# Kernel tuning notes

Measured on AMD Instinct MI355X. Metric: run time of the kernel, lower is better.

Reference implementation:

```python
import jax, jax.numpy as jnp
import numpy as np

N, IN_CH, HID, OUT = 3072, 128, 256, 32
HEADS = 12


def setup_inputs() -> dict:
    key = jax.random.key(0)
    ks = jax.random.split(key, 16)

    def glorot(k, shape):
        fan_in, fan_out = shape[0], shape[-1]
        lim = float(np.sqrt(6.0 / (fan_in + fan_out)))
        return jax.random.uniform(k, shape, jnp.float32, -lim, lim)

    return {
        "x": jax.random.normal(ks[0], (N, IN_CH), jnp.float32),
        "attn_tensor": jax.random.normal(ks[1], (HEADS, N, N), jnp.float32),
        "edge_weight": jnp.ones((1,), jnp.float32),  # unused (use_edge_weight=False)
        "batch_idx": jnp.zeros((N,), jnp.int64),      # single graph
        # Conv2d(12,1,1) == per-head scalar mix
        "agg_w": jax.random.normal(ks[2], (HEADS,), jnp.float32) * 0.1,
        "agg_b": jnp.zeros((1,), jnp.float32),
        # GCNConv weights (x @ W then propagate, + bias)
        "W1": glorot(ks[3], (IN_CH, HID)), "b1": jnp.zeros((HID,), jnp.float32),
        "W2": glorot(ks[4], (HID, HID)),   "b2": jnp.zeros((HID,), jnp.float32),
        # final MLP: Linear -> ReLU -> LayerNorm -> Linear
        "lin1_W": glorot(ks[5], (HID, HID)), "lin1_b": jnp.zeros((HID,), jnp.float32),
        "ln_g": jnp.ones((HID,), jnp.float32), "ln_b": jnp.zeros((HID,), jnp.float32),
        "lin2_W": glorot(ks[6], (HID, OUT)), "lin2_b": jnp.zeros((OUT,), jnp.float32),
    }


def reference(x, attn_tensor, edge_weight, batch_idx,
              agg_w, agg_b, W1, b1, W2, b2,
              lin1_W, lin1_b, ln_g, ln_b, lin2_W, lin2_b):
    threshold = 0.0
    n = x.shape[0]

    # Conv2d(12,1,kernel_size=1): weighted sum over heads -> [N, N] score matrix
    agg = jnp.einsum('c,cij->ij', agg_w, attn_tensor) + agg_b[0]

    # thresholded adjacency (mask.nonzero() -> edge_index), kept dense in jax
    A = (agg > threshold).astype(x.dtype)  # A[s, t] = edge s->t

    # PyG gcn_norm with add_remaining_self_loops (binary weights -> diag = 1)
    eye = jnp.eye(n, dtype=x.dtype)
    A_hat = A * (1.0 - eye) + eye
    deg = A_hat.sum(axis=0)                        # in-degree at target nodes
    dinv = jnp.where(deg > 0, jax.lax.rsqrt(deg), 0.0)
    A_norm = dinv[:, None] * A_hat * dinv[None, :]  # norm = dinv[src] * dinv[dst]

    # GCNConv 1: out[t] = sum_s A_norm[s,t] (x W)[s] + b
    h = jnp.einsum('st,sd->td', A_norm, x @ W1) + b1
    h = jax.nn.relu(h)
    # GCNConv 2
    h = jnp.einsum('st,sd->td', A_norm, h @ W2) + b2

    # global_mean_pool over batch_idx (single graph here)
    bi = batch_idx.astype(jnp.int32)
    sums = jax.ops.segment_sum(h, bi, num_segments=1)
    counts = jax.ops.segment_sum(jnp.ones((n,), h.dtype), bi, num_segments=1)
    g = sums / counts[:, None]

    # Linear -> ReLU -> LayerNorm -> Linear
    z = jax.nn.relu(g @ lin1_W + lin1_b)
    mu = z.mean(axis=-1, keepdims=True)
    var = ((z - mu) ** 2).mean(axis=-1, keepdims=True)
    z = (z - mu) * jax.lax.rsqrt(var + 1e-5) * ln_g + ln_b
    out = z @ lin2_W + lin2_b
    return out
```

## Files before the change

kernel.cpp:

```cpp
#include <hip/hip_runtime.h>
#include <hip/hip_bf16.h>

#define NN     3072
#define NWORDS 48
#define INCH   128
#define HID    256
#define NHEADS 12
#define PLANE  9437184LL

typedef __attribute__((ext_vector_type(8))) short     s16x8;
typedef __attribute__((ext_vector_type(4))) float     f32x4;
typedef __attribute__((ext_vector_type(8))) unsigned short u16x8;

__device__ inline unsigned short bf16_rne(float f) {
    unsigned int u = __float_as_uint(f);
    u += 0x7FFFu + ((u >> 16) & 1u);
    return (unsigned short)(u >> 16);
}

__global__ __launch_bounds__(256) void k_adj(const float* __restrict__ attn,
                                             const float* __restrict__ agg_w,
                                             const float* __restrict__ agg_b,
                                             unsigned long long* __restrict__ mask,
                                             unsigned long long* __restrict__ maskT) {
    __shared__ unsigned short chunk[4][64];
    const int w = threadIdx.x >> 6, l = threadIdx.x & 63;
    const int t0 = (blockIdx.x % 48) * 64;
    const int s0 = (blockIdx.x / 48) * 64;
    const int t = t0 + l;

    float wc[NHEADS];
#pragma unroll
    for (int c = 0; c < NHEADS; ++c) wc[c] = agg_w[c];
    const float bias = agg_b[0];

    unsigned int colchunk = 0;
#pragma unroll 2
    for (int i = 0; i < 16; ++i) {
        const int s = s0 + w * 16 + i;
        const float* p = attn + (long long)s * NN + t;
        float acc = bias;
#pragma unroll
        for (int c = 0; c < NHEADS; ++c)
            acc = fmaf(wc[c], p[(long long)c * PLANE], acc);
        bool pred = (acc > 0.0f) || (s == t);
        unsigned long long word = __ballot(pred);
        if (l == 0) mask[s * NWORDS + (t0 >> 6)] = word;
        colchunk |= (pred ? 1u : 0u) << i;
    }
    chunk[w][l] = (unsigned short)colchunk;
    __syncthreads();
    if (threadIdx.x < 64) {
        unsigned long long m = (unsigned long long)chunk[0][threadIdx.x]
                             | ((unsigned long long)chunk[1][threadIdx.x] << 16)
                             | ((unsigned long long)chunk[2][threadIdx.x] << 32)
                             | ((unsigned long long)chunk[3][threadIdx.x] << 48);
        maskT[(long long)(t0 + threadIdx.x) * NWORDS + (s0 >> 6)] = m;
    }
}

__global__ __launch_bounds__(256) void k_dinv(const unsigned long long* __restrict__ maskT,
                                              float* __restrict__ dinv,
                                              unsigned short* __restrict__ dinvb) {
    int t = blockIdx.x * 256 + threadIdx.x;
    const unsigned long long* row = maskT + (long long)t * NWORDS;
    int deg = 0;
#pragma unroll
    for (int w = 0; w < NWORDS; ++w) deg += __popcll(row[w]);
    float di = rsqrtf((float)deg);
    dinv[t] = di;
    dinvb[t] = bf16_rne(di);
}

__global__ __launch_bounds__(256) void k_fused(const unsigned long long* __restrict__ mask,
                                               const float* __restrict__ dinv,
                                               const float* __restrict__ x,
                                               const float* __restrict__ W1,
                                               float* __restrict__ w2sum,
                                               unsigned short* __restrict__ y1t) {
    if (blockIdx.x < 768) {
        const int w = threadIdx.x >> 6, l = threadIdx.x & 63;
        const int s = blockIdx.x * 4 + w;
        unsigned long long myword = (l < NWORDS) ? mask[s * NWORDS + l] : 0ULL;
        float acc = 0.0f;
#pragma unroll 8
        for (int j = 0; j < NWORDS; ++j) {
            unsigned long long wj = __shfl(myword, j);
            float dv = dinv[j * 64 + l];
            acc += ((wj >> l) & 1ULL) ? dv : 0.0f;
        }
#pragma unroll
        for (int o = 1; o < 64; o <<= 1) acc += __shfl_xor(acc, o);
        if (l == 0) w2sum[s] = dinv[s] * acc;
    } else {
        __shared__ float xs[8][INCH];
        int s0 = (blockIdx.x - 768) * 8;
        for (int i = threadIdx.x; i < 8 * INCH; i += 256)
            xs[i >> 7][i & 127] = x[s0 * INCH + i];
        __syncthreads();
        int d = threadIdx.x;
        float acc[8] = {0, 0, 0, 0, 0, 0, 0, 0};
        for (int k = 0; k < INCH; ++k) {
            float w = W1[k * HID + d];
#pragma unroll
            for (int r = 0; r < 8; ++r) acc[r] = fmaf(xs[r][k], w, acc[r]);
        }
        u16x8 v;
#pragma unroll
        for (int r = 0; r < 8; ++r) v[r] = bf16_rne(acc[r]);
        *(u16x8*)(y1t + (long long)d * NN + s0) = v;
    }
}

__global__ __launch_bounds__(256) void k_prop(const unsigned long long* __restrict__ maskT,
                                              const unsigned short* __restrict__ dinvb,
                                              const unsigned short* __restrict__ y1t,
                                              float* __restrict__ partials) {
    const int w = threadIdx.x >> 6, l = threadIdx.x & 63;
    const int lr = l & 15, lg = l >> 4;
    const int t0 = blockIdx.x * 64 + w * 16;
    const int d0 = blockIdx.y * 128;
    const int z  = blockIdx.z;

    const unsigned long long* mrow = maskT + (long long)(t0 + lr) * NWORDS + z * 12;

    const unsigned short* B[8];
#pragma unroll
    for (int n = 0; n < 8; ++n)
        B[n] = y1t + (long long)(d0 + n * 16 + lr) * NN;

    f32x4 acc[8];
#pragma unroll
    for (int n = 0; n < 8; ++n) acc[n] = (f32x4){0.f, 0.f, 0.f, 0.f};

#pragma unroll 2
    for (int kw = 0; kw < 12; ++kw) {
        unsigned long long word = mrow[kw];
#pragma unroll
        for (int half = 0; half < 2; ++half) {
            const int k0 = z * 768 + kw * 64 + half * 32 + lg * 8;
            unsigned int bits = (unsigned int)((word >> (half * 32 + lg * 8)) & 0xFFULL);
            u16x8 dv = *(const u16x8*)(dinvb + k0);
            s16x8 av;
#pragma unroll
            for (int j = 0; j < 8; ++j)
                av[j] = ((bits >> j) & 1u) ? (short)dv[j] : (short)0;
#pragma unroll
            for (int n = 0; n < 8; ++n) {
                s16x8 bv = *(const s16x8*)(const void*)(B[n] + k0);
                acc[n] = __builtin_amdgcn_mfma_f32_16x16x32_bf16(av, bv, acc[n], 0, 0, 0);
            }
        }
    }

    const int trow = t0 + lg * 4;
#pragma unroll
    for (int n = 0; n < 8; ++n) {
        const int d = d0 + n * 16 + lr;
#pragma unroll
        for (int r = 0; r < 4; ++r)
            partials[((size_t)z * NN + trow + r) * HID + d] = acc[n][r];
    }
}

__global__ __launch_bounds__(256) void k_vred(const float* __restrict__ partials,
                                              const float* __restrict__ dinv,
                                              const float* __restrict__ b1,
                                              const float* __restrict__ w2sum,
                                              float* __restrict__ vp) {
    const int b = blockIdx.x, d = threadIdx.x;
    const float bb = b1[d];
    float vacc = 0.0f;
#pragma unroll
    for (int i = 0; i < 8; ++i) {
        const int t = b * 8 + i;
        float ssum = partials[((size_t)0 * NN + t) * HID + d]
                   + partials[((size_t)1 * NN + t) * HID + d]
                   + partials[((size_t)2 * NN + t) * HID + d]
                   + partials[((size_t)3 * NN + t) * HID + d];
        float h = fmaxf(fmaf(dinv[t], ssum, bb), 0.0f);
        vacc = fmaf(w2sum[t], h, vacc);
    }
    vp[b * HID + d] = vacc;
}

__global__ __launch_bounds__(256) void k_head(const float* __restrict__ vp,
                                              const float* __restrict__ W2,
                                              const float* __restrict__ b2,
                                              const float* __restrict__ l1W,
                                              const float* __restrict__ l1b,
                                              const float* __restrict__ lng,
                                              const float* __restrict__ lnb,
                                              const float* __restrict__ l2W,
                                              const float* __restrict__ l2b,
                                              float* __restrict__ out) {
    __shared__ float vs[HID], gs[HID], zs[HID], red[4];
    int d = threadIdx.x;
    float v = 0.0f;
    for (int c = 0; c < 384; ++c) v += vp[c * HID + d];
    vs[d] = v;
    __syncthreads();
    float a = 0.0f;
    for (int k = 0; k < HID; ++k) a = fmaf(vs[k], W2[k * HID + d], a);
    gs[d] = b2[d] + a * (1.0f / 3072.0f);
    __syncthreads();
    float z1 = l1b[d];
    for (int k = 0; k < HID; ++k) z1 = fmaf(gs[k], l1W[k * HID + d], z1);
    z1 = fmaxf(z1, 0.0f);
    float sum = z1;
    for (int o = 1; o < 64; o <<= 1) sum += __shfl_xor(sum, o);
    if ((d & 63) == 0) red[d >> 6] = sum;
    __syncthreads();
    float mu = (red[0] + red[1] + red[2] + red[3]) * (1.0f / 256.0f);
    __syncthreads();
    float diff = z1 - mu, sq = diff * diff;
    for (int o = 1; o < 64; o <<= 1) sq += __shfl_xor(sq, o);
    if ((d & 63) == 0) red[d >> 6] = sq;
    __syncthreads();
    float var = (red[0] + red[1] + red[2] + red[3]) * (1.0f / 256.0f);
    float zn = diff * rsqrtf(var + 1e-5f) * lng[d] + lnb[d];
    zs[d] = zn;
    __syncthreads();
    if (d < 32) {
        float o = l2b[d];
        for (int k = 0; k < HID; ++k) o = fmaf(zs[k], l2W[k * 32 + d], o);
        out[d] = o;
    }
}

extern "C" void kernel_launch(void* const* d_in, const int* in_sizes, int n_in,
                              void* d_out, int out_size, void* d_ws, size_t ws_size,
                              hipStream_t stream) {
    const float* x     = (const float*)d_in[0];
    const float* attn  = (const float*)d_in[1];
    const float* agg_w = (const float*)d_in[4];
    const float* agg_b = (const float*)d_in[5];
    const float* W1    = (const float*)d_in[6];
    const float* b1    = (const float*)d_in[7];
    const float* W2    = (const float*)d_in[8];
    const float* b2    = (const float*)d_in[9];
    const float* l1W   = (const float*)d_in[10];
    const float* l1b   = (const float*)d_in[11];
    const float* lng   = (const float*)d_in[12];
    const float* lnb   = (const float*)d_in[13];
    const float* l2W   = (const float*)d_in[14];
    const float* l2b   = (const float*)d_in[15];
    float* out = (float*)d_out;

    char* ws = (char*)d_ws;
    size_t off = 0;
    auto alloc = [&](size_t bytes) -> void* {
        off = (off + 255) & ~(size_t)255;
        void* p = ws + off;
        off += bytes;
        return p;
    };
    unsigned long long* mask  = (unsigned long long*)alloc((size_t)NN * NWORDS * 8);
    unsigned long long* maskT = (unsigned long long*)alloc((size_t)NN * NWORDS * 8);
    float*          dinv  = (float*)alloc((size_t)NN * 4);
    unsigned short* dinvb = (unsigned short*)alloc((size_t)NN * 2);
    float*          w2sum = (float*)alloc((size_t)NN * 4);
    unsigned short* y1t   = (unsigned short*)alloc((size_t)HID * NN * 2);
    float*          part  = (float*)alloc((size_t)4 * NN * HID * 4);
    float*          vp    = (float*)alloc((size_t)384 * HID * 4);

    hipLaunchKernelGGL(k_adj,   dim3(2304), dim3(256), 0, stream, attn, agg_w, agg_b, mask, maskT);
    hipLaunchKernelGGL(k_dinv,  dim3(12),   dim3(256), 0, stream, maskT, dinv, dinvb);
    hipLaunchKernelGGL(k_fused, dim3(1152), dim3(256), 0, stream, mask, dinv, x, W1, w2sum, y1t);
    hipLaunchKernelGGL(k_prop,  dim3(48, 2, 4), dim3(256), 0, stream, maskT, dinvb, y1t, part);
    hipLaunchKernelGGL(k_vred,  dim3(384),  dim3(256), 0, stream, part, dinv, b1, w2sum, vp);
    hipLaunchKernelGGL(k_head,  dim3(1),    dim3(256), 0, stream,
                       vp, W2, b2, l1W, l1b, lng, lnb, l2W, l2b, out);
}
```

Before: 227.0 us.

## Drop row-major mask, vectorize adjacency build, fuse y1 and w2sum into other kernels

```diff
diff --git a/kernel.cpp b/kernel.cpp
--- a/kernel.cpp
+++ b/kernel.cpp
@@ -2,7 +2,7 @@
 #include <hip/hip_bf16.h>
 
 #define NN     3072
-#define NWORDS 48
+#define NW32   96
 #define INCH   128
 #define HID    256
 #define NHEADS 12
@@ -11,6 +11,7 @@
 typedef __attribute__((ext_vector_type(8))) short     s16x8;
 typedef __attribute__((ext_vector_type(4))) float     f32x4;
 typedef __attribute__((ext_vector_type(8))) unsigned short u16x8;
+typedef __attribute__((ext_vector_type(4))) unsigned int   u32x4;
 
 __device__ inline unsigned short bf16_rne(float f) {
     unsigned int u = __float_as_uint(f);
@@ -18,83 +19,59 @@
     return (unsigned short)(u >> 16);
 }
 
-__global__ __launch_bounds__(256) void k_adj(const float* __restrict__ attn,
-                                             const float* __restrict__ agg_w,
-                                             const float* __restrict__ agg_b,
-                                             unsigned long long* __restrict__ mask,
-                                             unsigned long long* __restrict__ maskT) {
-    __shared__ unsigned short chunk[4][64];
-    const int w = threadIdx.x >> 6, l = threadIdx.x & 63;
-    const int t0 = (blockIdx.x % 48) * 64;
-    const int s0 = (blockIdx.x / 48) * 64;
-    const int t = t0 + l;
-
-    float wc[NHEADS];
-#pragma unroll
-    for (int c = 0; c < NHEADS; ++c) wc[c] = agg_w[c];
-    const float bias = agg_b[0];
-
-    unsigned int colchunk = 0;
+__global__ __launch_bounds__(256) void k_adj_y1(const float* __restrict__ attn,
+                                                const float* __restrict__ agg_w,
+                                                const float* __restrict__ agg_b,
+                                                const float* __restrict__ x,
+                                                const float* __restrict__ W1,
+                                                unsigned int* __restrict__ maskT32,
+                                                unsigned short* __restrict__ y1t) {
+    __shared__ unsigned int chunkU[4][64];
+    __shared__ float xs[8][INCH];
+
+    if (blockIdx.x < 1152) {
+        const int w = threadIdx.x >> 6, l = threadIdx.x & 63;
+        const int t0 = (blockIdx.x % 12) * 256;
+        const int s0 = (blockIdx.x / 12) * 32;
+        const int tb = t0 + 4 * l;
+
+        float wc[NHEADS];
+#pragma unroll
+        for (int c = 0; c < NHEADS; ++c) wc[c] = agg_w[c];
+        const float bias = agg_b[0];
+
+        const float* base = attn + (long long)(s0 + 8 * w) * NN + tb;
+        unsigned int colb = 0;
 #pragma unroll 2
-    for (int i = 0; i < 16; ++i) {
-        const int s = s0 + w * 16 + i;
-        const float* p = attn + (long long)s * NN + t;
-        float acc = bias;
-#pragma unroll
-        for (int c = 0; c < NHEADS; ++c)
-            acc = fmaf(wc[c], p[(long long)c * PLANE], acc);
-        bool pred = (acc > 0.0f) || (s == t);
-        unsigned long long word = __ballot(pred);
-        if (l == 0) mask[s * NWORDS + (t0 >> 6)] = word;
-        colchunk |= (pred ? 1u : 0u) << i;
-    }
-    chunk[w][l] = (unsigned short)colchunk;
-    __syncthreads();
-    if (threadIdx.x < 64) {
-        unsigned long long m = (unsigned long long)chunk[0][threadIdx.x]
-                             | ((unsigned long long)chunk[1][threadIdx.x] << 16)
-                             | ((unsigned long long)chunk[2][threadIdx.x] << 32)
-                             | ((unsigned long long)chunk[3][threadIdx.x] << 48);
-        maskT[(long long)(t0 + threadIdx.x) * NWORDS + (s0 >> 6)] = m;
-    }
-}
-
-__global__ __launch_bounds__(256) void k_dinv(const unsigned long long* __restrict__ maskT,
-                                              float* __restrict__ dinv,
-                                              unsigned short* __restrict__ dinvb) {
-    int t = blockIdx.x * 256 + threadIdx.x;
-    const unsigned long long* row = maskT + (long long)t * NWORDS;
-    int deg = 0;
-#pragma unroll
-    for (int w = 0; w < NWORDS; ++w) deg += __popcll(row[w]);
-    float di = rsqrtf((float)deg);
-    dinv[t] = di;
-    dinvb[t] = bf16_rne(di);
-}
-
-__global__ __launch_bounds__(256) void k_fused(const unsigned long long* __restrict__ mask,
-                                               const float* __restrict__ dinv,
-                                               const float* __restrict__ x,
-                                               const float* __restrict__ W1,
-                                               float* __restrict__ w2sum,
-                                               unsigned short* __restrict__ y1t) {
-    if (blockIdx.x < 768) {
-        const int w = threadIdx.x >> 6, l = threadIdx.x & 63;
-        const int s = blockIdx.x * 4 + w;
-        unsigned long long myword = (l < NWORDS) ? mask[s * NWORDS + l] : 0ULL;
-        float acc = 0.0f;
-#pragma unroll 8
-        for (int j = 0; j < NWORDS; ++j) {
-            unsigned long long wj = __shfl(myword, j);
-            float dv = dinv[j * 64 + l];
-            acc += ((wj >> l) & 1ULL) ? dv : 0.0f;
-        }
-#pragma unroll
-        for (int o = 1; o < 64; o <<= 1) acc += __shfl_xor(acc, o);
-        if (l == 0) w2sum[s] = dinv[s] * acc;
+        for (int i = 0; i < 8; ++i) {
+            const int s = s0 + 8 * w + i;
+            const float* ps = base + (long long)i * NN;
+            f32x4 acc = {bias, bias, bias, bias};
+#pragma unroll
+            for (int c = 0; c < NHEADS; ++c) {
+                f32x4 v = *(const f32x4*)(ps + c * PLANE);
+                acc[0] = fmaf(wc[c], v[0], acc[0]);
+                acc[1] = fmaf(wc[c], v[1], acc[1]);
+                acc[2] = fmaf(wc[c], v[2], acc[2]);
+                acc[3] = fmaf(wc[c], v[3], acc[3]);
+            }
+            unsigned int bset = 0;
+            bset |= (acc[0] > 0.0f || s == tb + 0) ? (1u << i)        : 0u;
+            bset |= (acc[1] > 0.0f || s == tb + 1) ? (1u << (8 + i))  : 0u;
+            bset |= (acc[2] > 0.0f || s == tb + 2) ? (1u << (16 + i)) : 0u;
+            bset |= (acc[3] > 0.0f || s == tb + 3) ? (1u << (24 + i)) : 0u;
+            colb |= bset;
+        }
+        chunkU[w][l] = colb;
+        __syncthreads();
+        const int l2 = threadIdx.x >> 2, j = threadIdx.x & 3;
+        unsigned int word =  ((chunkU[0][l2] >> (8 * j)) & 0xFFu)
+                          | (((chunkU[1][l2] >> (8 * j)) & 0xFFu) << 8)
+                          | (((chunkU[2][l2] >> (8 * j)) & 0xFFu) << 16)
+                          | (((chunkU[3][l2] >> (8 * j)) & 0xFFu) << 24);
+        maskT32[(long long)(t0 + threadIdx.x) * NW32 + (s0 >> 5)] = word;
     } else {
-        __shared__ float xs[8][INCH];
-        int s0 = (blockIdx.x - 768) * 8;
+        int s0 = (blockIdx.x - 1152) * 8;
         for (int i = threadIdx.x; i < 8 * INCH; i += 256)
             xs[i >> 7][i & 127] = x[s0 * INCH + i];
         __syncthreads();
@@ -112,63 +89,112 @@
     }
 }
 
-__global__ __launch_bounds__(256) void k_prop(const unsigned long long* __restrict__ maskT,
+__global__ __launch_bounds__(256) void k_dinv(const unsigned int* __restrict__ maskT32,
+                                              float* __restrict__ dinv,
+                                              unsigned short* __restrict__ dinvb) {
+    int t = blockIdx.x * 256 + threadIdx.x;
+    const u32x4* row = (const u32x4*)(maskT32 + (long long)t * NW32);
+    int deg = 0;
+#pragma unroll
+    for (int i = 0; i < 24; ++i) {
+        u32x4 v = row[i];
+        deg += __popc(v[0]) + __popc(v[1]) + __popc(v[2]) + __popc(v[3]);
+    }
+    float di = rsqrtf((float)deg);
+    dinv[t] = di;
+    dinvb[t] = bf16_rne(di);
+}
+
+__global__ __launch_bounds__(256) void k_prop(const unsigned int* __restrict__ maskT32,
                                               const unsigned short* __restrict__ dinvb,
                                               const unsigned short* __restrict__ y1t,
-                                              float* __restrict__ partials) {
-    const int w = threadIdx.x >> 6, l = threadIdx.x & 63;
-    const int lr = l & 15, lg = l >> 4;
-    const int t0 = blockIdx.x * 64 + w * 16;
-    const int d0 = blockIdx.y * 128;
-    const int z  = blockIdx.z;
-
-    const unsigned long long* mrow = maskT + (long long)(t0 + lr) * NWORDS + z * 12;
-
-    const unsigned short* B[8];
-#pragma unroll
-    for (int n = 0; n < 8; ++n)
-        B[n] = y1t + (long long)(d0 + n * 16 + lr) * NN;
-
-    f32x4 acc[8];
-#pragma unroll
-    for (int n = 0; n < 8; ++n) acc[n] = (f32x4){0.f, 0.f, 0.f, 0.f};
+                                              const float* __restrict__ dinv,
+                                              float* __restrict__ partials,
+                                              float* __restrict__ w2p) {
+    if (blockIdx.x < 384) {
+        const int w = threadIdx.x >> 6, l = threadIdx.x & 63;
+        const int lr = l & 15, lg = l >> 4;
+        const int t0 = (blockIdx.x % 48) * 64 + w * 16;
+        const int d0 = ((blockIdx.x / 48) % 2) * 128;
+        const int z  = blockIdx.x / 96;
+
+        const unsigned long long* mrow =
+            (const unsigned long long*)(maskT32 + (long long)(t0 + lr) * NW32) + z * 12;
+
+        const unsigned short* B[8];
+#pragma unroll
+        for (int n = 0; n < 8; ++n)
+            B[n] = y1t + (long long)(d0 + n * 16 + lr) * NN;
+
+        f32x4 acc[8];
+#pragma unroll
+        for (int n = 0; n < 8; ++n) acc[n] = (f32x4){0.f, 0.f, 0.f, 0.f};
 
 #pragma unroll 2
-    for (int kw = 0; kw < 12; ++kw) {
-        unsigned long long word = mrow[kw];
-#pragma unroll
-        for (int half = 0; half < 2; ++half) {
-            const int k0 = z * 768 + kw * 64 + half * 32 + lg * 8;
-            unsigned int bits = (unsigned int)((word >> (half * 32 + lg * 8)) & 0xFFULL);
-            u16x8 dv = *(const u16x8*)(dinvb + k0);
-            s16x8 av;
-#pragma unroll
-            for (int j = 0; j < 8; ++j)
-                av[j] = ((bits >> j) & 1u) ? (short)dv[j] : (short)0;
-#pragma unroll
-            for (int n = 0; n < 8; ++n) {
-                s16x8 bv = *(const s16x8*)(const void*)(B[n] + k0);
-                acc[n] = __builtin_amdgcn_mfma_f32_16x16x32_bf16(av, bv, acc[n], 0, 0, 0);
+        for (int kw = 0; kw < 12; ++kw) {
+            unsigned long long word = mrow[kw];
+#pragma unroll
+            for (int half = 0; half < 2; ++half) {
+                const int k0 = z * 768 + kw * 64 + half * 32 + lg * 8;
+                unsigned int bits = (unsigned int)((word >> (half * 32 + lg * 8)) & 0xFFULL);
+                u16x8 dv = *(const u16x8*)(dinvb + k0);
+                s16x8 av;
+#pragma unroll
+                for (int j = 0; j < 8; ++j)
+                    av[j] = ((bits >> j) & 1u) ? (short)dv[j] : (short)0;
+#pragma unroll
+                for (int n = 0; n < 8; ++n) {
+                    s16x8 bv = *(const s16x8*)(const void*)(B[n] + k0);
+                    acc[n] = __builtin_amdgcn_mfma_f32_16x16x32_bf16(av, bv, acc[n], 0, 0, 0);
+                }
             }
         }
-    }
-
-    const int trow = t0 + lg * 4;
-#pragma unroll
-    for (int n = 0; n < 8; ++n) {
-        const int d = d0 + n * 16 + lr;
-#pragma unroll
-        for (int r = 0; r < 4; ++r)
-            partials[((size_t)z * NN + trow + r) * HID + d] = acc[n][r];
+
+        const int trow = t0 + lg * 4;
+#pragma unroll
+        for (int n = 0; n < 8; ++n) {
+            const int d = d0 + n * 16 + lr;
+#pragma unroll
+            for (int r = 0; r < 4; ++r)
+                partials[((size_t)z * NN + trow + r) * HID + d] = acc[n][r];
+        }
+    } else {
+        __shared__ float red[4][64];
+        const int r = blockIdx.x - 384;
+        const int wq = r % 48;
+        const int tc = r / 48;
+        const int wv = threadIdx.x >> 6, l = threadIdx.x & 63;
+        const unsigned long long* mt = (const unsigned long long*)maskT32;
+        float acc = 0.0f;
+#pragma unroll 4
+        for (int it = 0; it < 64; ++it) {
+            const int t = tc * 256 + wv * 64 + it;
+            unsigned long long word = mt[(long long)t * 48 + wq];
+            acc += ((word >> l) & 1ULL) ? dinv[t] : 0.0f;
+        }
+        red[wv][l] = acc;
+        __syncthreads();
+        if (threadIdx.x < 64)
+            w2p[tc * NN + wq * 64 + threadIdx.x] =
+                red[0][threadIdx.x] + red[1][threadIdx.x] + red[2][threadIdx.x] + red[3][threadIdx.x];
     }
 }
 
 __global__ __launch_bounds__(256) void k_vred(const float* __restrict__ partials,
                                               const float* __restrict__ dinv,
                                               const float* __restrict__ b1,
-                                              const float* __restrict__ w2sum,
+                                              const float* __restrict__ w2p,
                                               float* __restrict__ vp) {
+    __shared__ float w2s[8];
     const int b = blockIdx.x, d = threadIdx.x;
+    if (threadIdx.x < 8) {
+        const int t = b * 8 + threadIdx.x;
+        float a = 0.0f;
+#pragma unroll
+        for (int tc = 0; tc < 12; ++tc) a += w2p[tc * NN + t];
+        w2s[threadIdx.x] = dinv[t] * a;
+    }
+    __syncthreads();
     const float bb = b1[d];
     float vacc = 0.0f;
 #pragma unroll
@@ -179,7 +205,7 @@
                    + partials[((size_t)2 * NN + t) * HID + d]
                    + partials[((size_t)3 * NN + t) * HID + d];
         float h = fmaxf(fmaf(dinv[t], ssum, bb), 0.0f);
-        vacc = fmaf(w2sum[t], h, vacc);
+        vacc = fmaf(w2s[i], h, vacc);
     }
     vp[b * HID + d] = vacc;
 }
@@ -255,20 +281,20 @@
         off += bytes;
         return p;
     };
-    unsigned long long* mask  = (unsigned long long*)alloc((size_t)NN * NWORDS * 8);
-    unsigned long long* maskT = (unsigned long long*)alloc((size_t)NN * NWORDS * 8);
+    unsigned int*   maskT32 = (unsigned int*)alloc((size_t)NN * NW32 * 4);
     float*          dinv  = (float*)alloc((size_t)NN * 4);
     unsigned short* dinvb = (unsigned short*)alloc((size_t)NN * 2);
-    float*          w2sum = (float*)alloc((size_t)NN * 4);
+    float*          w2p   = (float*)alloc((size_t)12 * NN * 4);
     unsigned short* y1t   = (unsigned short*)alloc((size_t)HID * NN * 2);
     float*          part  = (float*)alloc((size_t)4 * NN * HID * 4);
     float*          vp    = (float*)alloc((size_t)384 * HID * 4);
 
-    hipLaunchKernelGGL(k_adj,   dim3(2304), dim3(256), 0, stream, attn, agg_w, agg_b, mask, maskT);
-    hipLaunchKernelGGL(k_dinv,  dim3(12),   dim3(256), 0, stream, maskT, dinv, dinvb);
-    hipLaunchKernelGGL(k_fused, dim3(1152), dim3(256), 0, stream, mask, dinv, x, W1, w2sum, y1t);
-    hipLaunchKernelGGL(k_prop,  dim3(48, 2, 4), dim3(256), 0, stream, maskT, dinvb, y1t, part);
-    hipLaunchKernelGGL(k_vred,  dim3(384),  dim3(256), 0, stream, part, dinv, b1, w2sum, vp);
-    hipLaunchKernelGGL(k_head,  dim3(1),    dim3(256), 0, stream,
+    hipLaunchKernelGGL(k_adj_y1, dim3(1536), dim3(256), 0, stream,
+                       attn, agg_w, agg_b, x, W1, maskT32, y1t);
+    hipLaunchKernelGGL(k_dinv,   dim3(12),   dim3(256), 0, stream, maskT32, dinv, dinvb);
+    hipLaunchKernelGGL(k_prop,   dim3(960),  dim3(256), 0, stream,
+                       maskT32, dinvb, y1t, dinv, part, w2p);
+    hipLaunchKernelGGL(k_vred,   dim3(384),  dim3(256), 0, stream, part, dinv, b1, w2p, vp);
+    hipLaunchKernelGGL(k_head,   dim3(1),    dim3(256), 0, stream,
                        vp, W2, b2, l1W, l1b, lng, lnb, l2W, l2b, out);
 }
```

New measurement: 191.7 us. 15.6% less time.
